# Performance work log

Hardware: AMD Instinct MI355X
Metric: run time of the kernel (lower is better)

## Reference

```python
import jax, jax.numpy as jnp
import numpy as np

B, H, W = 4, 64, 64
DIM, HEADS, HEAD = 768, 12, 64
WIN = 14
MLP_DIM = 4 * DIM
EPS = 1e-5


def _ln(x, g, b):
    mu = jnp.mean(x, axis=-1, keepdims=True)
    var = jnp.mean(jnp.square(x - mu), axis=-1, keepdims=True)
    return (x - mu) * jax.lax.rsqrt(var + EPS) * g + b


def _window_partition(x):
    Bb, Hh, Ww, C = x.shape
    pad_h = (WIN - Hh % WIN) % WIN
    pad_w = (WIN - Ww % WIN) % WIN
    x = jnp.pad(x, ((0, 0), (0, pad_h), (0, pad_w), (0, 0)))
    Hp, Wp = Hh + pad_h, Ww + pad_w
    x = x.reshape(Bb, Hp // WIN, WIN, Wp // WIN, WIN, C)
    win = x.transpose(0, 1, 3, 2, 4, 5).reshape(-1, WIN, WIN, C)
    return win, (Hp, Wp)


def _window_unpartition(win, pad_hw, hw):
    Hp, Wp = pad_hw
    Hh, Ww = hw
    Bb = win.shape[0] // (Hp * Wp // WIN // WIN)
    x = win.reshape(Bb, Hp // WIN, Wp // WIN, WIN, WIN, -1)
    x = x.transpose(0, 1, 3, 2, 4, 5).reshape(Bb, Hp, Wp, -1)
    return x[:, :Hh, :Ww, :]


def _attention(xw, qkv_w, qkv_b, proj_w, proj_b, rel_pos_h, rel_pos_w):
    Bw = xw.shape[0]
    N = WIN * WIN
    qkv = xw.reshape(Bw, N, DIM) @ qkv_w + qkv_b            # [Bw, N, 3*DIM]
    qkv = qkv.reshape(Bw, N, 3, HEADS, HEAD)
    qkv = qkv.transpose(2, 0, 3, 1, 4).reshape(3, Bw * HEADS, N, HEAD)
    q, k, v = qkv[0], qkv[1], qkv[2]
    scale = HEAD ** -0.5
    attn = jnp.einsum('bqc,bkc->bqk', q * scale, k)         # [Bw*HEADS, N, N]
    # decomposed relative position bias (q_size == k_size => plain gather)
    idx = jnp.arange(WIN)[:, None] - jnp.arange(WIN)[None, :] + (WIN - 1)
    Rh = rel_pos_h[idx]
    Rw = rel_pos_w[idx]
    r_q = q.reshape(-1, WIN, WIN, HEAD)
    rel_h = jnp.einsum('bhwc,hkc->bhwk', r_q, Rh)
    rel_w = jnp.einsum('bhwc,wkc->bhwk', r_q, Rw)
    attn = attn.reshape(-1, WIN, WIN, WIN, WIN) + rel_h[..., None] + rel_w[..., None, :]
    attn = jax.nn.softmax(attn.reshape(-1, N, N), axis=-1)
    out = attn @ v                                          # [Bw*HEADS, N, HEAD]
    out = out.reshape(Bw, HEADS, WIN, WIN, HEAD).transpose(0, 2, 3, 1, 4)
    out = out.reshape(Bw, WIN, WIN, DIM)
    return out @ proj_w + proj_b


def setup_inputs() -> dict:
    key = jax.random.key(0)
    ks = jax.random.split(key, 8)
    s = 0.02
    return {
        'x': jax.random.normal(ks[0], (B, H, W, DIM), jnp.float32),
        'norm1_g': jnp.ones((DIM,), jnp.float32),
        'norm1_b': jnp.zeros((DIM,), jnp.float32),
        'qkv_w': jax.random.normal(ks[1], (DIM, 3 * DIM), jnp.float32) * s,
        'qkv_b': jnp.zeros((3 * DIM,), jnp.float32),
        'proj_w': jax.random.normal(ks[2], (DIM, DIM), jnp.float32) * s,
        'proj_b': jnp.zeros((DIM,), jnp.float32),
        'rel_pos_h': jax.random.normal(ks[3], (2 * WIN - 1, HEAD), jnp.float32) * s,
        'rel_pos_w': jax.random.normal(ks[4], (2 * WIN - 1, HEAD), jnp.float32) * s,
        'norm2_g': jnp.ones((DIM,), jnp.float32),
        'norm2_b': jnp.zeros((DIM,), jnp.float32),
        'mlp_w1': jax.random.normal(ks[5], (DIM, MLP_DIM), jnp.float32) * s,
        'mlp_b1': jnp.zeros((MLP_DIM,), jnp.float32),
        'mlp_w2': jax.random.normal(ks[6], (MLP_DIM, DIM), jnp.float32) * s,
        'mlp_b2': jnp.zeros((DIM,), jnp.float32),
    }


def reference(x, norm1_g, norm1_b, qkv_w, qkv_b, proj_w, proj_b,
              rel_pos_h, rel_pos_w, norm2_g, norm2_b,
              mlp_w1, mlp_b1, mlp_w2, mlp_b2):
    shortcut = x
    x = _ln(x, norm1_g, norm1_b)
    win, pad_hw = _window_partition(x)
    win = _attention(win, qkv_w, qkv_b, proj_w, proj_b, rel_pos_h, rel_pos_w)
    x = _window_unpartition(win, pad_hw, (H, W))
    x = shortcut + x
    y = _ln(x, norm2_g, norm2_b)
    y = jax.nn.gelu(y @ mlp_w1 + mlp_b1, approximate=False) @ mlp_w2 + mlp_b2
    return x + y
```

## Files before the change

kernel.cpp:

```cpp
#include <hip/hip_runtime.h>
#include <hip/hip_bf16.h>
#include <math.h>

#define DIMC 768
#define NHEADS 12
#define WINSZ 14
#define NTOK 196
#define TOKENS 16384

using bf = __hip_bfloat16;
typedef __attribute__((ext_vector_type(4))) float f32x4;
typedef __attribute__((ext_vector_type(8))) short bf16x8;

typedef __attribute__((address_space(3))) void lds_void_t;
typedef const __attribute__((address_space(1))) void gmem_void_t;

__device__ inline float bfu2f(ushort u) { return __uint_as_float((uint)u << 16); }
__device__ inline ushort f2bu(float f) {
    bf t = __float2bfloat16(f);
    return __builtin_bit_cast(ushort, t);
}

__global__ __launch_bounds__(256) void transpose_k(const float* __restrict__ in,
                                                   ushort* __restrict__ out, int R, int C) {
    long i = (long)blockIdx.x * 256 + threadIdx.x;
    if (i >= (long)R * C) return;
    int r = (int)(i / C), c = (int)(i % C);
    out[(long)c * R + r] = f2bu(in[i]);
}

__device__ inline float blk_sum(float v, float* wred, int tid) {
    for (int m = 32; m; m >>= 1) v += __shfl_xor(v, m);
    if ((tid & 63) == 0) wred[tid >> 6] = v;
    __syncthreads();
    float r = wred[0] + wred[1] + wred[2] + wred[3];
    __syncthreads();
    return r;
}

__global__ __launch_bounds__(256) void ln_k(const float* __restrict__ x, const float* __restrict__ g,
                                            const float* __restrict__ bb, ushort* __restrict__ out) {
    int row = blockIdx.x, tid = threadIdx.x;
    const float* xr = x + (size_t)row * DIMC;
    __shared__ float wred[4];
    float v0 = xr[tid], v1 = xr[tid + 256], v2 = xr[tid + 512];
    float mean = blk_sum(v0 + v1 + v2, wred, tid) * (1.f / 768.f);
    float d0 = v0 - mean, d1 = v1 - mean, d2 = v2 - mean;
    float var = blk_sum(d0 * d0 + d1 * d1 + d2 * d2, wred, tid) * (1.f / 768.f);
    float rs = rsqrtf(var + 1e-5f);
    ushort* o = out + (size_t)row * DIMC;
    o[tid]       = f2bu(d0 * rs * g[tid]       + bb[tid]);
    o[tid + 256] = f2bu(d1 * rs * g[tid + 256] + bb[tid + 256]);
    o[tid + 512] = f2bu(d2 * rs * g[tid + 512] + bb[tid + 512]);
}

enum { EPI_BIAS = 0, EPI_GELU = 1, EPI_PROJRES = 2, EPI_ACC = 3, EPI_RESOUT = 4 };

template <int EPI>
__global__ __launch_bounds__(256) void gemm_k(const ushort* __restrict__ A, int lda,
                                              const ushort* __restrict__ Bt, int ldb,
                                              const float* __restrict__ bias,
                                              ushort* __restrict__ outb,
                                              float* __restrict__ outf,
                                              const float* __restrict__ xorig,
                                              float* __restrict__ x2,
                                              int N, int K) {
    __shared__ ushort lA[128 * 32];
    __shared__ ushort lB[128 * 32];
    const int bm = blockIdx.y * 128, bn = blockIdx.x * 128;
    const int tid = threadIdx.x, wave = tid >> 6, lane = tid & 63;
    const int wy = wave >> 1, wx = wave & 1;
    const int lm = lane & 15, quad = lane >> 4;

    f32x4 acc[4][4];
#pragma unroll
    for (int r = 0; r < 4; ++r)
#pragma unroll
        for (int s = 0; s < 4; ++s) acc[r][s] = (f32x4){0.f, 0.f, 0.f, 0.f};

    const int c0 = wave * 2, c1 = wave * 2 + 1;
    const ushort* Ab = A + (size_t)(bm + (lane >> 2)) * lda + (lane & 3) * 8;
    const ushort* Bb = Bt + (size_t)(bn + (lane >> 2)) * ldb + (lane & 3) * 8;
    const size_t a16 = (size_t)16 * lda, b16 = (size_t)16 * ldb;

    for (int k0 = 0; k0 < K; k0 += 32) {
        __builtin_amdgcn_global_load_lds((gmem_void_t*)(Ab + (size_t)c0 * a16 + k0),
                                         (lds_void_t*)&lA[c0 * 512], 16, 0, 0);
        __builtin_amdgcn_global_load_lds((gmem_void_t*)(Ab + (size_t)c1 * a16 + k0),
                                         (lds_void_t*)&lA[c1 * 512], 16, 0, 0);
        __builtin_amdgcn_global_load_lds((gmem_void_t*)(Bb + (size_t)c0 * b16 + k0),
                                         (lds_void_t*)&lB[c0 * 512], 16, 0, 0);
        __builtin_amdgcn_global_load_lds((gmem_void_t*)(Bb + (size_t)c1 * b16 + k0),
                                         (lds_void_t*)&lB[c1 * 512], 16, 0, 0);
        __syncthreads();

        bf16x8 af[4], bv[4];
#pragma unroll
        for (int r = 0; r < 4; ++r)
            af[r] = *(const bf16x8*)&lA[(wy * 64 + r * 16 + lm) * 32 + quad * 8];
#pragma unroll
        for (int s = 0; s < 4; ++s)
            bv[s] = *(const bf16x8*)&lB[(wx * 64 + s * 16 + lm) * 32 + quad * 8];
#pragma unroll
        for (int r = 0; r < 4; ++r)
#pragma unroll
            for (int s = 0; s < 4; ++s)
                acc[r][s] = __builtin_amdgcn_mfma_f32_16x16x32_bf16(af[r], bv[s], acc[r][s], 0, 0, 0);
        __syncthreads();
    }

#pragma unroll
    for (int s = 0; s < 4; ++s) {
        int col = bn + wx * 64 + s * 16 + lm;
        float bvl = (EPI == EPI_ACC) ? 0.f : bias[col];
#pragma unroll
        for (int r = 0; r < 4; ++r) {
#pragma unroll
            for (int i = 0; i < 4; ++i) {
                int row = bm + wy * 64 + r * 16 + quad * 4 + i;
                float v = acc[r][s][i] + bvl;
                size_t idx = (size_t)row * N + col;
                if constexpr (EPI == EPI_BIAS) {
                    outb[idx] = f2bu(v);
                } else if constexpr (EPI == EPI_GELU) {
                    outb[idx] = f2bu(0.5f * v * (1.f + erff(v * 0.70710678118f)));
                } else if constexpr (EPI == EPI_PROJRES) {
                    x2[idx] = xorig[idx] + v;
                } else if constexpr (EPI == EPI_ACC) {
                    x2[idx] += v;
                } else {
                    outf[idx] = x2[idx] + v;
                }
            }
        }
    }
}

__global__ __launch_bounds__(256) void attn_k(const ushort* __restrict__ qkv,
                                              const float* __restrict__ qkvb,
                                              const float* __restrict__ relh,
                                              const float* __restrict__ relw,
                                              ushort* __restrict__ aout) {
    const int win = blockIdx.x / NHEADS, head = blockIdx.x % NHEADS;
    const int b = win / 25, wi = win % 25, wr = wi / 5, wc = wi % 5;
    const int hmax = (wr == 4) ? 8 : WINSZ, wmax = (wc == 4) ? 8 : WINSZ;
    const int hoff = head * 64;
    const int tid = threadIdx.x, wave = tid >> 6, lane = tid & 63;
    const int c = lane & 15, quad = lane >> 4;

    __shared__ ushort Ksw[224 * 64];
    __shared__ ushort vTs[64 * 232];
    __shared__ ushort wscr[4][640];

    for (int t = tid; t < 224 * 8; t += 256) {
        int n = t >> 3, ck = t & 7;
        int kh = n >> 4, kw = n & 15;
        union { uint4 u; ushort s[8]; } vals;
        if (kw < WINSZ) {
            if (kh < hmax && kw < wmax) {
                size_t tok = ((size_t)(b * 64 + wr * WINSZ + kh) * 64 + wc * WINSZ + kw);
                union { uint4 u; ushort s[8]; } raw;
                raw.u = *(const uint4*)(qkv + tok * 2304 + 768 + hoff + ck * 8);
#pragma unroll
                for (int j = 0; j < 8; ++j) vals.s[j] = f2bu(0.125f * bfu2f(raw.s[j]));
            } else {
#pragma unroll
                for (int j = 0; j < 8; ++j) vals.s[j] = f2bu(0.125f * qkvb[768 + hoff + ck * 8 + j]);
            }
        } else {
            vals.u = (uint4){0u, 0u, 0u, 0u};
        }
        *(uint4*)&Ksw[n * 64 + ((ck ^ (n & 7)) * 8)] = vals.u;
    }
    for (int u = tid; u < 64 * 28; u += 256) {
        int d = u / 28, kc = u % 28;
        union { uint4 u4; ushort s[8]; } vals;
#pragma unroll
        for (int j = 0; j < 8; ++j) {
            int n = kc * 8 + j, kh = n >> 4, kw = n & 15;
            ushort v = 0;
            if (kw < WINSZ) {
                if (kh < hmax && kw < wmax) {
                    size_t tok = ((size_t)(b * 64 + wr * WINSZ + kh) * 64 + wc * WINSZ + kw);
                    v = qkv[tok * 2304 + 1536 + hoff + d];
                } else {
                    v = f2bu(qkvb[1536 + hoff + d]);
                }
            }
            vals.s[j] = v;
        }
        *(uint4*)&vTs[d * 232 + kc * 8] = vals.u4;
    }
    __syncthreads();

    bf16x8 rhB[2][2], rwB[2][2];
#pragma unroll
    for (int nt = 0; nt < 2; ++nt) {
        int j = nt * 16 + c; if (j > 26) j = 26;
#pragma unroll
        for (int ks = 0; ks < 2; ++ks) {
            const float* ph = relh + (size_t)j * 64 + ks * 32 + quad * 8;
            const float* pw = relw + (size_t)j * 64 + ks * 32 + quad * 8;
            bf16x8 h, w;
#pragma unroll
            for (int e = 0; e < 8; ++e) {
                h[e] = (short)f2bu(ph[e]);
                w[e] = (short)f2bu(pw[e]);
            }
            rhB[nt][ks] = h; rwB[nt][ks] = w;
        }
    }

    ushort* scr = &wscr[wave][0];
    const int lane48 = lane & 48;

    for (int qh = wave; qh < hmax; qh += 4) {
        int qw = c < wmax ? c : (wmax - 1);
        size_t qtok = ((size_t)(b * 64 + wr * WINSZ + qh) * 64 + wc * WINSZ + qw);
        bf16x8 aq0 = *(const bf16x8*)(qkv + qtok * 2304 + hoff + quad * 8);
        bf16x8 aq1 = *(const bf16x8*)(qkv + qtok * 2304 + hoff + 32 + quad * 8);

        f32x4 z = (f32x4){0.f, 0.f, 0.f, 0.f};
        f32x4 dh0 = __builtin_amdgcn_mfma_f32_16x16x32_bf16(aq0, rhB[0][0], z, 0, 0, 0);
        dh0 = __builtin_amdgcn_mfma_f32_16x16x32_bf16(aq1, rhB[0][1], dh0, 0, 0, 0);
        f32x4 dh1 = __builtin_amdgcn_mfma_f32_16x16x32_bf16(aq0, rhB[1][0], z, 0, 0, 0);
        dh1 = __builtin_amdgcn_mfma_f32_16x16x32_bf16(aq1, rhB[1][1], dh1, 0, 0, 0);
        f32x4 dw0 = __builtin_amdgcn_mfma_f32_16x16x32_bf16(aq0, rwB[0][0], z, 0, 0, 0);
        dw0 = __builtin_amdgcn_mfma_f32_16x16x32_bf16(aq1, rwB[0][1], dw0, 0, 0, 0);
        f32x4 dw1 = __builtin_amdgcn_mfma_f32_16x16x32_bf16(aq0, rwB[1][0], z, 0, 0, 0);
        dw1 = __builtin_amdgcn_mfma_f32_16x16x32_bf16(aq1, rwB[1][1], dw1, 0, 0, 0);

#pragma unroll
        for (int i = 0; i < 4; ++i) {
            scr[(quad * 4 + i) * 28 + c] = f2bu(dh0[i]);
            if (c < 12) scr[(quad * 4 + i) * 28 + 16 + c] = f2bu(dh1[i]);
        }

        float bw[4];
#pragma unroll
        for (int i = 0; i < 4; ++i) {
            int m = quad * 4 + i;
            int j = m - c + 13; int jc = j < 0 ? 0 : j;
            int addr = (lane48 | (jc & 15)) << 2;
            int t0 = __builtin_amdgcn_ds_bpermute(addr, __float_as_int(dw0[i]));
            int t1 = __builtin_amdgcn_ds_bpermute(addr, __float_as_int(dw1[i]));
            bw[i] = (jc >= 16) ? __int_as_float(t1) : __int_as_float(t0);
        }

        f32x4 s[14];
#pragma unroll
        for (int kh = 0; kh < 14; ++kh) {
            int n = kh * 16 + c;
            int n7 = n & 7;
            bf16x8 kb0 = *(const bf16x8*)&Ksw[n * 64 + ((0 * 4 + quad) ^ n7) * 8];
            bf16x8 kb1 = *(const bf16x8*)&Ksw[n * 64 + ((1 * 4 + quad) ^ n7) * 8];
            f32x4 acc = __builtin_amdgcn_mfma_f32_16x16x32_bf16(aq0, kb0, z, 0, 0, 0);
            acc = __builtin_amdgcn_mfma_f32_16x16x32_bf16(aq1, kb1, acc, 0, 0, 0);
            int jstar = qh + 13 - kh;
#pragma unroll
            for (int i = 0; i < 4; ++i) {
                float dh = bfu2f(scr[(quad * 4 + i) * 28 + jstar]);
                float v = acc[i] + dh + bw[i];
                acc[i] = (c < WINSZ) ? v : -1e30f;
            }
            s[kh] = acc;
        }

        float inv[4];
#pragma unroll
        for (int i = 0; i < 4; ++i) {
            float mx = s[0][i];
#pragma unroll
            for (int kh = 1; kh < 14; ++kh) mx = fmaxf(mx, s[kh][i]);
            mx = fmaxf(mx, __shfl_xor(mx, 1));
            mx = fmaxf(mx, __shfl_xor(mx, 2));
            mx = fmaxf(mx, __shfl_xor(mx, 4));
            mx = fmaxf(mx, __shfl_xor(mx, 8));
            float sum = 0.f;
#pragma unroll
            for (int kh = 0; kh < 14; ++kh) {
                float e = __expf(s[kh][i] - mx);
                s[kh][i] = e;
                sum += e;
            }
            sum += __shfl_xor(sum, 1);
            sum += __shfl_xor(sum, 2);
            sum += __shfl_xor(sum, 4);
            sum += __shfl_xor(sum, 8);
            inv[i] = 1.f / sum;
        }

        f32x4 o[4] = {z, z, z, z};
#pragma unroll
        for (int cc = 0; cc < 7; ++cc) {
#pragma unroll
            for (int i = 0; i < 4; ++i) {
                scr[(quad * 4 + i) * 40 + c]      = f2bu(s[2 * cc][i] * inv[i]);
                scr[(quad * 4 + i) * 40 + 16 + c] = f2bu(s[2 * cc + 1][i] * inv[i]);
            }
            bf16x8 ap = *(const bf16x8*)&scr[c * 40 + quad * 8];
#pragma unroll
            for (int vt = 0; vt < 4; ++vt) {
                bf16x8 vb = *(const bf16x8*)&vTs[(vt * 16 + c) * 232 + cc * 32 + quad * 8];
                o[vt] = __builtin_amdgcn_mfma_f32_16x16x32_bf16(ap, vb, o[vt], 0, 0, 0);
            }
        }

#pragma unroll
        for (int i = 0; i < 4; ++i) {
            int qwp = quad * 4 + i;
            if (qwp < wmax) {
                size_t otok = ((size_t)(b * 64 + wr * WINSZ + qh) * 64 + wc * WINSZ + qwp);
#pragma unroll
                for (int vt = 0; vt < 4; ++vt)
                    aout[otok * 768 + hoff + vt * 16 + c] = f2bu(o[vt][i]);
            }
        }
    }
}

extern "C" void kernel_launch(void* const* d_in, const int* in_sizes, int n_in,
                              void* d_out, int out_size, void* d_ws, size_t ws_size,
                              hipStream_t stream) {
    const float* x      = (const float*)d_in[0];
    const float* n1g    = (const float*)d_in[1];
    const float* n1b    = (const float*)d_in[2];
    const float* qkv_w  = (const float*)d_in[3];
    const float* qkv_b  = (const float*)d_in[4];
    const float* proj_w = (const float*)d_in[5];
    const float* proj_b = (const float*)d_in[6];
    const float* relh   = (const float*)d_in[7];
    const float* relw   = (const float*)d_in[8];
    const float* n2g    = (const float*)d_in[9];
    const float* n2b    = (const float*)d_in[10];
    const float* w1     = (const float*)d_in[11];
    const float* b1     = (const float*)d_in[12];
    const float* w2     = (const float*)d_in[13];
    const float* b2     = (const float*)d_in[14];
    float* out = (float*)d_out;

    char* ws = (char*)d_ws;
    size_t off = 0;
    auto alloc = [&](size_t bytes) -> void* {
        void* p = ws + off;
        off += (bytes + 255) & ~(size_t)255;
        return p;
    };

    ushort* lnbuf  = (ushort*)alloc((size_t)TOKENS * DIMC * 2);
    ushort* qkvbuf = (ushort*)alloc((size_t)TOKENS * 2304 * 2);
    float* x2      = (float*)alloc((size_t)TOKENS * DIMC * 4);
    ushort* qkvT   = (ushort*)alloc((size_t)2304 * 768 * 2);
    ushort* projT  = (ushort*)alloc((size_t)768 * 768 * 2);
    ushort* w1T    = (ushort*)alloc((size_t)3072 * 768 * 2);
    ushort* w2T    = (ushort*)alloc((size_t)768 * 3072 * 2);
    ushort* aout   = lnbuf;
    ushort* hc     = qkvbuf;

    transpose_k<<<(768 * 2304 + 255) / 256, 256, 0, stream>>>(qkv_w, qkvT, 768, 2304);
    transpose_k<<<(768 * 768 + 255) / 256, 256, 0, stream>>>(proj_w, projT, 768, 768);
    transpose_k<<<(768 * 3072 + 255) / 256, 256, 0, stream>>>(w1, w1T, 768, 3072);
    transpose_k<<<(3072 * 768 + 255) / 256, 256, 0, stream>>>(w2, w2T, 3072, 768);

    ln_k<<<TOKENS, 256, 0, stream>>>(x, n1g, n1b, lnbuf);

    dim3 gq(2304 / 128, TOKENS / 128);
    gemm_k<EPI_BIAS><<<gq, 256, 0, stream>>>(lnbuf, DIMC, qkvT, DIMC, qkv_b, qkvbuf,
                                             nullptr, nullptr, nullptr, 2304, DIMC);

    attn_k<<<100 * NHEADS, 256, 0, stream>>>(qkvbuf, qkv_b, relh, relw, aout);

    dim3 gp(DIMC / 128, TOKENS / 128);
    gemm_k<EPI_PROJRES><<<gp, 256, 0, stream>>>(aout, DIMC, projT, DIMC, proj_b, nullptr,
                                                nullptr, x, x2, DIMC, DIMC);

    ln_k<<<TOKENS, 256, 0, stream>>>(x2, n2g, n2b, lnbuf);

    dim3 gh(1536 / 128, TOKENS / 128);
    for (int c = 0; c < 2; ++c) {
        gemm_k<EPI_GELU><<<gh, 256, 0, stream>>>(lnbuf, DIMC, w1T + (size_t)c * 1536 * 768, DIMC,
                                                 b1 + c * 1536, hc, nullptr, nullptr, nullptr,
                                                 1536, DIMC);
        if (c == 0)
            gemm_k<EPI_ACC><<<gp, 256, 0, stream>>>(hc, 1536, w2T + (size_t)c * 1536, 3072,
                                                    b2, nullptr, nullptr, nullptr, x2, DIMC, 1536);
        else
            gemm_k<EPI_RESOUT><<<gp, 256, 0, stream>>>(hc, 1536, w2T + (size_t)c * 1536, 3072,
                                                       b2, nullptr, out, nullptr, x2, DIMC, 1536);
    }
}
```

Baseline: 774.0 us.

## Double the GEMM K-step and vectorize swizzled V staging in attention

The GEMM main loop now handles 64 K elements per iteration. It stages two 32-wide LDS tiles per operand, so each pair of barriers covers twice the MFMA work. In the attention kernel, V is loaded with 16-byte vector reads per token and scattered into an XOR-swizzled transposed LDS layout, replacing scalar gathers. The 1/8 query scale moves from the K staging into an fmaf on the scores, which removes per-element convert work. The cost is double the GEMM LDS footprint, which may reduce occupancy, plus more scattered 2-byte LDS stores when building V.

```diff
diff --git a/kernel.cpp b/kernel.cpp
--- a/kernel.cpp
+++ b/kernel.cpp
@@ -65,8 +65,10 @@
                                               const float* __restrict__ xorig,
                                               float* __restrict__ x2,
                                               int N, int K) {
-    __shared__ ushort lA[128 * 32];
-    __shared__ ushort lB[128 * 32];
+    __shared__ ushort lA0[128 * 32];
+    __shared__ ushort lA1[128 * 32];
+    __shared__ ushort lB0[128 * 32];
+    __shared__ ushort lB1[128 * 32];
     const int bm = blockIdx.y * 128, bn = blockIdx.x * 128;
     const int tid = threadIdx.x, wave = tid >> 6, lane = tid & 63;
     const int wy = wave >> 1, wx = wave & 1;
@@ -83,29 +85,43 @@
     const ushort* Bb = Bt + (size_t)(bn + (lane >> 2)) * ldb + (lane & 3) * 8;
     const size_t a16 = (size_t)16 * lda, b16 = (size_t)16 * ldb;
 
-    for (int k0 = 0; k0 < K; k0 += 32) {
+    for (int k0 = 0; k0 < K; k0 += 64) {
         __builtin_amdgcn_global_load_lds((gmem_void_t*)(Ab + (size_t)c0 * a16 + k0),
-                                         (lds_void_t*)&lA[c0 * 512], 16, 0, 0);
+                                         (lds_void_t*)&lA0[c0 * 512], 16, 0, 0);
+        __builtin_amdgcn_global_load_lds((gmem_void_t*)(Ab + (size_t)c0 * a16 + k0 + 32),
+                                         (lds_void_t*)&lA1[c0 * 512], 16, 0, 0);
         __builtin_amdgcn_global_load_lds((gmem_void_t*)(Ab + (size_t)c1 * a16 + k0),
-                                         (lds_void_t*)&lA[c1 * 512], 16, 0, 0);
+                                         (lds_void_t*)&lA0[c1 * 512], 16, 0, 0);
+        __builtin_amdgcn_global_load_lds((gmem_void_t*)(Ab + (size_t)c1 * a16 + k0 + 32),
+                                         (lds_void_t*)&lA1[c1 * 512], 16, 0, 0);
         __builtin_amdgcn_global_load_lds((gmem_void_t*)(Bb + (size_t)c0 * b16 + k0),
-                                         (lds_void_t*)&lB[c0 * 512], 16, 0, 0);
+                                         (lds_void_t*)&lB0[c0 * 512], 16, 0, 0);
+        __builtin_amdgcn_global_load_lds((gmem_void_t*)(Bb + (size_t)c0 * b16 + k0 + 32),
+                                         (lds_void_t*)&lB1[c0 * 512], 16, 0, 0);
         __builtin_amdgcn_global_load_lds((gmem_void_t*)(Bb + (size_t)c1 * b16 + k0),
-                                         (lds_void_t*)&lB[c1 * 512], 16, 0, 0);
+                                         (lds_void_t*)&lB0[c1 * 512], 16, 0, 0);
+        __builtin_amdgcn_global_load_lds((gmem_void_t*)(Bb + (size_t)c1 * b16 + k0 + 32),
+                                         (lds_void_t*)&lB1[c1 * 512], 16, 0, 0);
         __syncthreads();
 
-        bf16x8 af[4], bv[4];
+        bf16x8 af0[4], af1[4], bv0[4], bv1[4];
+#pragma unroll
+        for (int r = 0; r < 4; ++r) {
+            af0[r] = *(const bf16x8*)&lA0[(wy * 64 + r * 16 + lm) * 32 + quad * 8];
+            af1[r] = *(const bf16x8*)&lA1[(wy * 64 + r * 16 + lm) * 32 + quad * 8];
+        }
+#pragma unroll
+        for (int s = 0; s < 4; ++s) {
+            bv0[s] = *(const bf16x8*)&lB0[(wx * 64 + s * 16 + lm) * 32 + quad * 8];
+            bv1[s] = *(const bf16x8*)&lB1[(wx * 64 + s * 16 + lm) * 32 + quad * 8];
+        }
 #pragma unroll
         for (int r = 0; r < 4; ++r)
-            af[r] = *(const bf16x8*)&lA[(wy * 64 + r * 16 + lm) * 32 + quad * 8];
-#pragma unroll
-        for (int s = 0; s < 4; ++s)
-            bv[s] = *(const bf16x8*)&lB[(wx * 64 + s * 16 + lm) * 32 + quad * 8];
-#pragma unroll
-        for (int r = 0; r < 4; ++r)
-#pragma unroll
-            for (int s = 0; s < 4; ++s)
-                acc[r][s] = __builtin_amdgcn_mfma_f32_16x16x32_bf16(af[r], bv[s], acc[r][s], 0, 0, 0);
+#pragma unroll
+            for (int s = 0; s < 4; ++s) {
+                acc[r][s] = __builtin_amdgcn_mfma_f32_16x16x32_bf16(af0[r], bv0[s], acc[r][s], 0, 0, 0);
+                acc[r][s] = __builtin_amdgcn_mfma_f32_16x16x32_bf16(af1[r], bv1[s], acc[r][s], 0, 0, 0);
+            }
         __syncthreads();
     }
 
@@ -149,47 +165,45 @@
     const int c = lane & 15, quad = lane >> 4;
 
     __shared__ ushort Ksw[224 * 64];
-    __shared__ ushort vTs[64 * 232];
+    __shared__ ushort vTs[64 * 264];
     __shared__ ushort wscr[4][640];
 
     for (int t = tid; t < 224 * 8; t += 256) {
         int n = t >> 3, ck = t & 7;
         int kh = n >> 4, kw = n & 15;
+        uint4 vals;
+        if (kw < WINSZ && kh < hmax && kw < wmax) {
+            size_t tok = ((size_t)(b * 64 + wr * WINSZ + kh) * 64 + wc * WINSZ + kw);
+            vals = *(const uint4*)(qkv + tok * 2304 + 768 + hoff + ck * 8);
+        } else if (kw < WINSZ) {
+            union { uint4 u; ushort s[8]; } tmp;
+#pragma unroll
+            for (int j = 0; j < 8; ++j) tmp.s[j] = f2bu(qkvb[768 + hoff + ck * 8 + j]);
+            vals = tmp.u;
+        } else {
+            vals = (uint4){0u, 0u, 0u, 0u};
+        }
+        *(uint4*)&Ksw[n * 64 + ((ck ^ (n & 7)) * 8)] = vals;
+    }
+    for (int t = tid; t < 224 * 8; t += 256) {
+        int n = t >> 3, dg = t & 7;
+        int kh = n >> 4, kw = n & 15;
         union { uint4 u; ushort s[8]; } vals;
-        if (kw < WINSZ) {
-            if (kh < hmax && kw < wmax) {
-                size_t tok = ((size_t)(b * 64 + wr * WINSZ + kh) * 64 + wc * WINSZ + kw);
-                union { uint4 u; ushort s[8]; } raw;
-                raw.u = *(const uint4*)(qkv + tok * 2304 + 768 + hoff + ck * 8);
-#pragma unroll
-                for (int j = 0; j < 8; ++j) vals.s[j] = f2bu(0.125f * bfu2f(raw.s[j]));
-            } else {
-#pragma unroll
-                for (int j = 0; j < 8; ++j) vals.s[j] = f2bu(0.125f * qkvb[768 + hoff + ck * 8 + j]);
-            }
+        if (kw < WINSZ && kh < hmax && kw < wmax) {
+            size_t tok = ((size_t)(b * 64 + wr * WINSZ + kh) * 64 + wc * WINSZ + kw);
+            vals.u = *(const uint4*)(qkv + tok * 2304 + 1536 + hoff + dg * 8);
+        } else if (kw < WINSZ) {
+#pragma unroll
+            for (int j = 0; j < 8; ++j) vals.s[j] = f2bu(qkvb[1536 + hoff + dg * 8 + j]);
         } else {
             vals.u = (uint4){0u, 0u, 0u, 0u};
         }
-        *(uint4*)&Ksw[n * 64 + ((ck ^ (n & 7)) * 8)] = vals.u;
-    }
-    for (int u = tid; u < 64 * 28; u += 256) {
-        int d = u / 28, kc = u % 28;
-        union { uint4 u4; ushort s[8]; } vals;
+        int kchunk = n >> 3;
 #pragma unroll
         for (int j = 0; j < 8; ++j) {
-            int n = kc * 8 + j, kh = n >> 4, kw = n & 15;
-            ushort v = 0;
-            if (kw < WINSZ) {
-                if (kh < hmax && kw < wmax) {
-                    size_t tok = ((size_t)(b * 64 + wr * WINSZ + kh) * 64 + wc * WINSZ + kw);
-                    v = qkv[tok * 2304 + 1536 + hoff + d];
-                } else {
-                    v = f2bu(qkvb[1536 + hoff + d]);
-                }
-            }
-            vals.s[j] = v;
-        }
-        *(uint4*)&vTs[d * 232 + kc * 8] = vals.u4;
+            int d = dg * 8 + j;
+            vTs[d * 264 + ((kchunk ^ dg) * 8) + (n & 7)] = vals.s[j];
+        }
     }
     __syncthreads();
 
@@ -260,7 +274,7 @@
 #pragma unroll
             for (int i = 0; i < 4; ++i) {
                 float dh = bfu2f(scr[(quad * 4 + i) * 28 + jstar]);
-                float v = acc[i] + dh + bw[i];
+                float v = fmaf(0.125f, acc[i], dh + bw[i]);
                 acc[i] = (c < WINSZ) ? v : -1e30f;
             }
             s[kh] = acc;
@@ -301,7 +315,9 @@
             bf16x8 ap = *(const bf16x8*)&scr[c * 40 + quad * 8];
 #pragma unroll
             for (int vt = 0; vt < 4; ++vt) {
-                bf16x8 vb = *(const bf16x8*)&vTs[(vt * 16 + c) * 232 + cc * 32 + quad * 8];
+                int d = vt * 16 + c;
+                int dgr = (d >> 3) & 7;
+                bf16x8 vb = *(const bf16x8*)&vTs[d * 264 + (((cc * 4 + quad) ^ dgr) * 8)];
                 o[vt] = __builtin_amdgcn_mfma_f32_16x16x32_bf16(ap, vb, o[vt], 0, 0, 0);
             }
         }
```

Result: faster. 710.5 us (-8.2%).
